# Kernel tuning notes

Hardware: AMD Instinct MI355X
Metric: run time of the kernel (lower is better)

## Reference

```python
import jax, jax.numpy as jnp
import numpy as np

MIN_BIN_WIDTH = 1e-3
MIN_BIN_HEIGHT = 1e-3
MIN_DERIVATIVE = 1e-3
TAIL_BOUND = 1.0
N_POS = 2097152
N_CHANNELS = 8
N_BINS = 128
DEFAULT_INIT = float(np.log(np.exp(1.0 - MIN_DERIVATIVE) - 1.0))


def setup_inputs() -> dict:
    key = jax.random.key(0)
    k1, k2, k3, k4 = jax.random.split(key, 4)
    # positions rescaled to roughly [-1, 1]; include slight tail overshoot
    x = jax.random.uniform(k1, (N_POS, N_CHANNELS), minval=-1.1, maxval=1.1, dtype=jnp.float32)
    uw = DEFAULT_INIT + 0.1 * jax.random.normal(k2, (N_CHANNELS, N_BINS), dtype=jnp.float32)
    uh = DEFAULT_INIT + 0.1 * jax.random.normal(k3, (N_CHANNELS, N_BINS), dtype=jnp.float32)
    ud = DEFAULT_INIT + 0.1 * jax.random.normal(k4, (N_CHANNELS, N_BINS - 1), dtype=jnp.float32)
    return {"x": x, "unnormalized_widths": uw, "unnormalized_heights": uh,
            "unnormalized_derivatives": ud}


def _bin_edges(unnormalized, min_size, left, right):
    # softmax-normalized sizes with a minimum bin size, cumsum -> knot locations
    n_bins = unnormalized.shape[-1]
    sizes = jax.nn.softmax(unnormalized, axis=-1)
    sizes = min_size + (1.0 - min_size * n_bins) * sizes
    cum = jnp.cumsum(sizes, axis=-1)
    cum = jnp.pad(cum, ((0, 0), (1, 0)))
    cum = (right - left) * cum + left
    cum = cum.at[..., 0].set(left).at[..., -1].set(right)
    sizes = cum[..., 1:] - cum[..., :-1]
    return sizes, cum


def _log_prob(x, uw, uh, ud):
    left, right = -TAIL_BOUND, TAIL_BOUND
    bottom, top = -TAIL_BOUND, TAIL_BOUND
    C = uw.shape[0]

    widths, cumwidths = _bin_edges(uw * 10.0, MIN_BIN_WIDTH, left, right)      # (C,B),(C,B+1)
    heights, cumheights = _bin_edges(uh * 10.0, MIN_BIN_HEIGHT, bottom, top)   # (C,B),(C,B+1)
    ud_pad = jnp.pad(ud, ((0, 0), (1, 1)), constant_values=DEFAULT_INIT)       # linear tails
    derivatives = MIN_DERIVATIVE + jax.nn.softplus(ud_pad)                      # (C,B+1)
    delta = heights / widths                                                    # (C,B)

    inside = (x >= left) & (x <= right)
    xc = jnp.clip(x, bottom, top)  # inverse pass searches over cumheights

    edges = cumheights.at[:, -1].add(1e-6)
    # per-channel bin search, memory-light searchsorted
    idx = jax.vmap(lambda e, v: jnp.searchsorted(e, v, side='right'),
                   in_axes=(0, 1), out_axes=1)(edges, xc) - 1                   # (N,C)
    idx = jnp.clip(idx, 0, widths.shape[-1] - 1)

    ch = jnp.arange(C)[None, :]
    icw = cumwidths[ch, idx]
    ibw = widths[ch, idx]
    ich = cumheights[ch, idx]
    ih = heights[ch, idx]
    idl = delta[ch, idx]
    d0 = derivatives[ch, idx]
    d1 = derivatives[ch, idx + 1]

    # quadratic inverse solve (Durkan et al. rational-quadratic spline)
    dy = xc - ich
    t = d0 + d1 - 2.0 * idl
    a = dy * t + ih * (idl - d0)
    b = ih * d0 - dy * t
    c = -idl * dy
    disc = jnp.maximum(b * b - 4.0 * a * c, 0.0)
    root = (2.0 * c) / (-b - jnp.sqrt(disc))
    theta_1m = root * (1.0 - root)
    denom = idl + t * theta_1m
    der_num = (idl ** 2) * (d1 * root ** 2 + 2.0 * idl * theta_1m + d0 * (1.0 - root) ** 2)
    logabsdet = jnp.log(der_num) - 2.0 * jnp.log(denom)
    logdet = jnp.where(inside, -logabsdet, 0.0)  # identity tails -> logdet 0
    return np.log(0.5).astype(np.float32) + logdet


def reference(x, unnormalized_widths, unnormalized_heights, unnormalized_derivatives):
    return _log_prob(x, unnormalized_widths, unnormalized_heights, unnormalized_derivatives)
```

## Files before the change

kernel.cpp:

```cpp
#include <hip/hip_runtime.h>
#include <math.h>


#define NB 128
#define NCH 8
#define NSLOT 1024
#define PACK_B 4128
#define HINT_B 20640
#define TAB_FLOATS 7212

typedef float v2f __attribute__((ext_vector_type(2)));

static __device__ inline unsigned short f2h(float v) {
    union { _Float16 h; unsigned short u; } c;
    c.h = (_Float16)v;
    return c.u;
}
static __device__ inline float h16lo(unsigned u) {
    union { unsigned short s; _Float16 h; } c; c.s = (unsigned short)(u & 0xffffu);
    return (float)c.h;
}
static __device__ inline float h16hi(unsigned u) {
    union { unsigned short s; _Float16 h; } c; c.s = (unsigned short)(u >> 16);
    return (float)c.h;
}

__global__ __launch_bounds__(128) void spline_precompute(
    const float* __restrict__ uw, const float* __restrict__ uh,
    const float* __restrict__ ud, float* __restrict__ ws)
{
    const int c = blockIdx.x;
    const int i = threadIdx.x;
    __shared__ float red[128];
    __shared__ float scan[128];
    __shared__ float cum[129];
    __shared__ float wdt[128];
    __shared__ float sdv[129];
    const float DEFAULT_INIT = logf(expf(1.0f - 1e-3f) - 1.0f);

    float v = uw[c * NB + i] * 10.0f;
    red[i] = v; __syncthreads();
    #pragma unroll
    for (int s = 64; s >= 1; s >>= 1) { if (i < s) red[i] = fmaxf(red[i], red[i + s]); __syncthreads(); }
    float ex = expf(v - red[0]);
    __syncthreads();
    red[i] = ex; __syncthreads();
    #pragma unroll
    for (int s = 64; s >= 1; s >>= 1) { if (i < s) red[i] += red[i + s]; __syncthreads(); }
    float sz = 1e-3f + (1.0f - 1e-3f * NB) * (ex / red[0]);
    __syncthreads();
    scan[i] = sz;
    for (int off = 1; off < NB; off <<= 1) {
        __syncthreads();
        float t = (i >= off) ? scan[i - off] : 0.0f;
        __syncthreads();
        scan[i] += t;
    }
    __syncthreads();
    if (i == 0) cum[0] = -1.0f;
    cum[i + 1] = (i == NB - 1) ? 1.0f : fmaf(2.0f, scan[i], -1.0f);
    __syncthreads();
    wdt[i] = cum[i + 1] - cum[i];
    __syncthreads();

    v = uh[c * NB + i] * 10.0f;
    red[i] = v; __syncthreads();
    #pragma unroll
    for (int s = 64; s >= 1; s >>= 1) { if (i < s) red[i] = fmaxf(red[i], red[i + s]); __syncthreads(); }
    ex = expf(v - red[0]);
    __syncthreads();
    red[i] = ex; __syncthreads();
    #pragma unroll
    for (int s = 64; s >= 1; s >>= 1) { if (i < s) red[i] += red[i + s]; __syncthreads(); }
    sz = 1e-3f + (1.0f - 1e-3f * NB) * (ex / red[0]);
    __syncthreads();
    scan[i] = sz;
    for (int off = 1; off < NB; off <<= 1) {
        __syncthreads();
        float t = (i >= off) ? scan[i - off] : 0.0f;
        __syncthreads();
        scan[i] += t;
    }
    __syncthreads();
    if (i == 0) cum[0] = -1.0f;
    cum[i + 1] = (i == NB - 1) ? 1.0f : fmaf(2.0f, scan[i], -1.0f);

    float u0 = (i == 0) ? DEFAULT_INIT : ud[c * (NB - 1) + i - 1];
    sdv[i] = 1e-3f + log1pf(expf(u0));
    if (i == NB - 1) sdv[NB] = 1e-3f + log1pf(expf(DEFAULT_INIT));
    __syncthreads();

    float hh  = cum[i + 1] - cum[i];
    float idl = hh / wdt[i];
    float d0v = sdv[i], d1v = sdv[i + 1];
    float Tv  = d0v + d1v - 2.0f * idl;
    const int o = c * 129 + i;

    ws[o] = cum[i];
    if (i == NB - 1) ws[c * 129 + NB] = 1.0f + 1e-6f;

    uint4* g_pk = reinterpret_cast<uint4*>(reinterpret_cast<char*>(ws) + PACK_B);
    unsigned dld0 = (unsigned)f2h(idl) | ((unsigned)f2h(d0v) << 16);
    g_pk[o] = make_uint4(__float_as_uint(hh), dld0, (unsigned)f2h(Tv), 0u);
    if (i == NB - 1)
        g_pk[o + 1] = make_uint4(__float_as_uint(1.0f),
                                 (unsigned)f2h(1.0f) | ((unsigned)f2h(1.0f) << 16),
                                 0u, 0u);

    unsigned char* g_hint = reinterpret_cast<unsigned char*>(ws) + HINT_B;
    for (int s = i; s < NSLOT + 1; s += NB) {
        float left = (float)s * (2.0f / NSLOT) - 1.0f;
        int k = 0;
        #pragma unroll
        for (int st = 64; st >= 1; st >>= 1) {
            int t = k + st;
            if (cum[t] <= left) k = t;
        }
        g_hint[c * (NSLOT + 1) + s] = (unsigned char)k;
    }
}

__global__ __launch_bounds__(256, 4) void spline_main(
    const float4* __restrict__ x4, float4* __restrict__ out4,
    const float* __restrict__ ws, int npair)
{
    __shared__ __align__(16) float tab[TAB_FLOATS];
    {
        float4* dst = reinterpret_cast<float4*>(tab);
        const float4* src = reinterpret_cast<const float4*>(ws);
        for (int t = threadIdx.x; t < TAB_FLOATS / 4; t += 256) dst[t] = src[t];
    }
    __syncthreads();
    const float* eg = tab;
    const uint4* pk4 = reinterpret_cast<const uint4*>(
        reinterpret_cast<const char*>(tab) + PACK_B);
    const unsigned char* hint = reinterpret_cast<const unsigned char*>(tab) + HINT_B;

    const float LOG_HALF = -0.6931471805599453f;
    const float LN2 = 0.6931471805599453f;
    const int tid = blockIdx.x * 256 + threadIdx.x;
    const int stride = gridDim.x * 256;

    float4 pfa, pfb;
    if (tid < npair) { pfa = x4[2 * tid]; pfb = x4[2 * tid + 1]; }

    for (int i = tid; i < npair; i += stride) {
        float4 xa = pfa, xb = pfb;
        int inx = i + stride;
        inx = (inx < npair) ? inx : i;
        pfa = x4[2 * inx];
        pfb = x4[2 * inx + 1];

        float xs[8] = {xa.x, xa.y, xa.z, xa.w, xb.x, xb.y, xb.z, xb.w};

        float xq[8];
        int kk[8];
        #pragma unroll
        for (int j = 0; j < 8; ++j) {
            float xc = __builtin_amdgcn_fmed3f(xs[j], -1.0f, 1.0f);
            xq[j] = xc;
            int s = (int)fmaf(xc, (float)(NSLOT / 2), (float)(NSLOT / 2));
            kk[j] = hint[j * (NSLOT + 1) + s];
        }

        float e0[8], e1[8];
        #pragma unroll
        for (int j = 0; j < 8; ++j) {
            const float* ej = eg + j * 129 + kk[j];
            e0[j] = ej[0];
            e1[j] = ej[1];
        }

        uint4 pr[8];
        float dyv[8], lm[8];
        #pragma unroll
        for (int j = 0; j < 8; ++j) {
            bool adv = (e1[j] <= xq[j]);
            int k2 = kk[j] + (adv ? 1 : 0);
            float elo = adv ? e1[j] : e0[j];
            dyv[j] = xq[j] - elo;
            lm[j] = (xs[j] == xq[j]) ? LN2 : 0.0f;
            pr[j] = pk4[j * 129 + k2];
        }

        float rs[8];
        #pragma unroll
        for (int jj = 0; jj < 4; ++jj) {
            v2f h  = {__uint_as_float(pr[jj].x), __uint_as_float(pr[jj + 4].x)};
            v2f dl = {h16lo(pr[jj].y), h16lo(pr[jj + 4].y)};
            v2f d0 = {h16hi(pr[jj].y), h16hi(pr[jj + 4].y)};
            v2f T  = {h16lo(pr[jj].z), h16lo(pr[jj + 4].z)};
            v2f dy = {dyv[jj], dyv[jj + 4]};
            const v2f four = {4.0f, 4.0f};
            const v2f zz = {0.0f, 0.0f};

            v2f dyt  = dy * T;
            v2f sdd  = dl - d0;
            v2f a    = __builtin_elementwise_fma(h, sdd, dyt);
            v2f b    = __builtin_elementwise_fma(h, d0, -dyt);
            v2f cp   = dl * dy;
            v2f ac   = a * cp;
            v2f disc = __builtin_elementwise_max(
                           __builtin_elementwise_fma(four, ac, b * b), zz);
            v2f sq   = {__builtin_amdgcn_sqrtf(disc.x),
                        __builtin_amdgcn_sqrtf(disc.y)};
            v2f t2   = b + sq;
            v2f uu   = cp + cp;
            v2f t2s  = t2 * t2;
            v2f tu   = T * uu;
            v2f tmu  = t2 - uu;
            v2f denb = __builtin_elementwise_fma(tu, tmu, dl * t2s);
            v2f numf = h * denb;
            v2f den  = (dl * sq) * t2s;

            float va = __fdividef(numf.x, den.x);
            float vb = __fdividef(numf.y, den.y);
            rs[jj]     = fmaf(lm[jj],     __log2f(va), LOG_HALF);
            rs[jj + 4] = fmaf(lm[jj + 4], __log2f(vb), LOG_HALF);
        }

        out4[2 * i]     = make_float4(rs[0], rs[1], rs[2], rs[3]);
        out4[2 * i + 1] = make_float4(rs[4], rs[5], rs[6], rs[7]);
    }
}

extern "C" void kernel_launch(void* const* d_in, const int* in_sizes, int n_in,
                              void* d_out, int out_size, void* d_ws, size_t ws_size,
                              hipStream_t stream) {
    const float* x  = (const float*)d_in[0];
    const float* uw = (const float*)d_in[1];
    const float* uh = (const float*)d_in[2];
    const float* ud = (const float*)d_in[3];
    float* ws = (float*)d_ws;

    spline_precompute<<<NCH, NB, 0, stream>>>(uw, uh, ud, ws);

    const int npair = out_size / 8;
    spline_main<<<2048, 256, 0, stream>>>(
        (const float4*)x, (float4*)d_out, ws, npair);
}
```

Before: 40.53 us.

## Shrink shared-memory table to 12-byte records and raise occupancy to 6 waves

Packs each per-bin record into three 32-bit words instead of a padded uint4, drops the sentinel bin and extra hint slot, and shrinks the LDS table. The launch bound rises from 4 to 6 blocks per SIMD-equivalent to increase occupancy, limiting register budget. The division is replaced by a difference of two log2 calls. Loads become three scalar LDS reads instead of one 128-bit read, and register pressure may cause spills under the tighter launch bound.

```diff
diff --git a/kernel.cpp b/kernel.cpp
--- a/kernel.cpp
+++ b/kernel.cpp
@@ -6,8 +6,8 @@
 #define NCH 8
 #define NSLOT 1024
 #define PACK_B 4128
-#define HINT_B 20640
-#define TAB_FLOATS 7212
+#define HINT_B 16416
+#define TAB_FLOATS 6152
 
 typedef float v2f __attribute__((ext_vector_type(2)));
 
@@ -94,21 +94,18 @@
     float idl = hh / wdt[i];
     float d0v = sdv[i], d1v = sdv[i + 1];
     float Tv  = d0v + d1v - 2.0f * idl;
-    const int o = c * 129 + i;
-
-    ws[o] = cum[i];
+
+    ws[c * 129 + i] = cum[i];
     if (i == NB - 1) ws[c * 129 + NB] = 1.0f + 1e-6f;
 
-    uint4* g_pk = reinterpret_cast<uint4*>(reinterpret_cast<char*>(ws) + PACK_B);
-    unsigned dld0 = (unsigned)f2h(idl) | ((unsigned)f2h(d0v) << 16);
-    g_pk[o] = make_uint4(__float_as_uint(hh), dld0, (unsigned)f2h(Tv), 0u);
-    if (i == NB - 1)
-        g_pk[o + 1] = make_uint4(__float_as_uint(1.0f),
-                                 (unsigned)f2h(1.0f) | ((unsigned)f2h(1.0f) << 16),
-                                 0u, 0u);
+    unsigned* g_pk = reinterpret_cast<unsigned*>(reinterpret_cast<char*>(ws) + PACK_B);
+    const int pw = (c * NB + i) * 3;
+    g_pk[pw]     = __float_as_uint(hh);
+    g_pk[pw + 1] = (unsigned)f2h(idl) | ((unsigned)f2h(d0v) << 16);
+    g_pk[pw + 2] = (unsigned)f2h(Tv);
 
     unsigned char* g_hint = reinterpret_cast<unsigned char*>(ws) + HINT_B;
-    for (int s = i; s < NSLOT + 1; s += NB) {
+    for (int s = i; s < NSLOT; s += NB) {
         float left = (float)s * (2.0f / NSLOT) - 1.0f;
         int k = 0;
         #pragma unroll
@@ -116,11 +113,11 @@
             int t = k + st;
             if (cum[t] <= left) k = t;
         }
-        g_hint[c * (NSLOT + 1) + s] = (unsigned char)k;
-    }
-}
-
-__global__ __launch_bounds__(256, 4) void spline_main(
+        g_hint[c * NSLOT + s] = (unsigned char)k;
+    }
+}
+
+__global__ __launch_bounds__(256, 6) void spline_main(
     const float4* __restrict__ x4, float4* __restrict__ out4,
     const float* __restrict__ ws, int npair)
 {
@@ -132,7 +129,7 @@
     }
     __syncthreads();
     const float* eg = tab;
-    const uint4* pk4 = reinterpret_cast<const uint4*>(
+    const unsigned* pku = reinterpret_cast<const unsigned*>(
         reinterpret_cast<const char*>(tab) + PACK_B);
     const unsigned char* hint = reinterpret_cast<const unsigned char*>(tab) + HINT_B;
 
@@ -160,7 +157,8 @@
             float xc = __builtin_amdgcn_fmed3f(xs[j], -1.0f, 1.0f);
             xq[j] = xc;
             int s = (int)fmaf(xc, (float)(NSLOT / 2), (float)(NSLOT / 2));
-            kk[j] = hint[j * (NSLOT + 1) + s];
+            s = (s > NSLOT - 1) ? NSLOT - 1 : s;
+            kk[j] = hint[j * NSLOT + s];
         }
 
         float e0[8], e1[8];
@@ -171,7 +169,7 @@
             e1[j] = ej[1];
         }
 
-        uint4 pr[8];
+        unsigned pw0[8], pw1[8], pw2[8];
         float dyv[8], lm[8];
         #pragma unroll
         for (int j = 0; j < 8; ++j) {
@@ -180,16 +178,19 @@
             float elo = adv ? e1[j] : e0[j];
             dyv[j] = xq[j] - elo;
             lm[j] = (xs[j] == xq[j]) ? LN2 : 0.0f;
-            pr[j] = pk4[j * 129 + k2];
+            const unsigned* p = pku + (j * NB + k2) * 3;
+            pw0[j] = p[0];
+            pw1[j] = p[1];
+            pw2[j] = p[2];
         }
 
         float rs[8];
         #pragma unroll
         for (int jj = 0; jj < 4; ++jj) {
-            v2f h  = {__uint_as_float(pr[jj].x), __uint_as_float(pr[jj + 4].x)};
-            v2f dl = {h16lo(pr[jj].y), h16lo(pr[jj + 4].y)};
-            v2f d0 = {h16hi(pr[jj].y), h16hi(pr[jj + 4].y)};
-            v2f T  = {h16lo(pr[jj].z), h16lo(pr[jj + 4].z)};
+            v2f h  = {__uint_as_float(pw0[jj]), __uint_as_float(pw0[jj + 4])};
+            v2f dl = {h16lo(pw1[jj]), h16lo(pw1[jj + 4])};
+            v2f d0 = {h16hi(pw1[jj]), h16hi(pw1[jj + 4])};
+            v2f T  = {h16lo(pw2[jj]), h16lo(pw2[jj + 4])};
             v2f dy = {dyv[jj], dyv[jj + 4]};
             const v2f four = {4.0f, 4.0f};
             const v2f zz = {0.0f, 0.0f};
@@ -213,10 +214,10 @@
             v2f numf = h * denb;
             v2f den  = (dl * sq) * t2s;
 
-            float va = __fdividef(numf.x, den.x);
-            float vb = __fdividef(numf.y, den.y);
-            rs[jj]     = fmaf(lm[jj],     __log2f(va), LOG_HALF);
-            rs[jj + 4] = fmaf(lm[jj + 4], __log2f(vb), LOG_HALF);
+            float la = __log2f(numf.x) - __log2f(den.x);
+            float lb = __log2f(numf.y) - __log2f(den.y);
+            rs[jj]     = fmaf(lm[jj],     la, LOG_HALF);
+            rs[jj + 4] = fmaf(lm[jj + 4], lb, LOG_HALF);
         }
 
         out4[2 * i]     = make_float4(rs[0], rs[1], rs[2], rs[3]);
```

New measurement: 40.05 us. Within noise of the previous version (-1.2%).
